# Kernel optimization log

Measured on AMD Instinct MI355X. Metric: run time of the kernel, lower is better.

The kernel has to match this reference:

```python
import jax, jax.numpy as jnp
import numpy as np

WIN = 7
HEADS = 3

def _relative_bias(window_size: int) -> jnp.ndarray:
    # Faithful reproduction of RelativeEmbeddings.__init__ (numpy handles negative
    # indices with wrap-around exactly like torch fancy indexing).
    rng = np.random.default_rng(0)
    B = rng.standard_normal((2 * window_size - 1, 2 * window_size - 1)).astype(np.float32)
    x = np.arange(1, window_size + 1, 1 / window_size)  # length window_size**2
    xi = (x[None, :] - x[:, None]).astype(np.int64)
    y = np.concatenate([np.arange(1, window_size + 1)] * window_size)
    yi = y[None, :] - y[:, None]
    return jnp.asarray(B[xi, yi])  # [w^2, w^2]


def setup_inputs() -> dict:
    key = jax.random.key(0)
    k0, k1, k2 = jax.random.split(key, 3)
    C = 96
    x = jax.random.normal(k0, (64, 3136, C), dtype=jnp.float32)
    w_qkv = jax.random.normal(k1, (C, 3 * C), dtype=jnp.float32) * 0.02
    b_qkv = jnp.zeros((3 * C,), dtype=jnp.float32)
    w_proj = jax.random.normal(k2, (C, C), dtype=jnp.float32) * 0.02
    b_proj = jnp.zeros((C,), dtype=jnp.float32)
    rel_bias = _relative_bias(WIN)
    return {"x": x, "w_qkv": w_qkv, "b_qkv": b_qkv, "w_proj": w_proj,
            "b_proj": b_proj, "rel_bias": rel_bias}


def reference(x, w_qkv, b_qkv, w_proj, b_proj, rel_bias):
    B, L, C = x.shape
    h = w = int(np.sqrt(L))
    m = WIN
    H = HEADS
    E = C // H
    scale = 1.0 / (E ** 0.5)

    qkv = x @ w_qkv + b_qkv                                   # [B, L, 3C]
    # torch rearrange: last dim layout is (H, E, K=3), spatial split into windows
    qkv = qkv.reshape(B, h // m, m, w // m, m, H, E, 3)
    qkv = qkv.transpose(0, 5, 1, 3, 2, 4, 6, 7)               # [B,H,hw,ww,m1,m2,E,3]
    qkv = qkv.reshape(B, H, h // m, w // m, m * m, E, 3)
    q, k, v = qkv[..., 0], qkv[..., 1], qkv[..., 2]           # [B,H,hw,ww,m^2,E]

    scores = jnp.einsum('bhxyqe,bhxyke->bhxyqk', q, k) * scale + rel_bias
    attn = jax.nn.softmax(scores, axis=-1)
    out = jnp.einsum('bhxyqk,bhxyke->bhxyqe', attn, v)        # [B,H,hw,ww,m^2,E]

    out = out.reshape(B, H, h // m, w // m, m, m, E)
    out = out.transpose(0, 2, 4, 3, 5, 1, 6).reshape(B, L, C)  # b (h m1) (w m2) (H E)
    return out @ w_proj + b_proj
```

## Files before the change

### kernel.cpp

```cpp
#include <hip/hip_runtime.h>

typedef unsigned int u32;
typedef __bf16 bf16_t;
typedef bf16_t bf16x8 __attribute__((ext_vector_type(8)));
typedef float f32x4 __attribute__((ext_vector_type(4)));

#define NB 64
#define GH 56
#define CC 96
#define NH 3
#define MM 7
#define WT 49
#define C3 288
#define LL 3136

static constexpr size_t ATTN_OFF = 0;
static constexpr size_t WQ_OFF   = (size_t)NB * LL * CC * 2;
static constexpr size_t WP_OFF   = WQ_OFF + 54 * 1024;
static constexpr size_t BR_OFF   = WP_OFF + 18 * 1024;

static __device__ __forceinline__ unsigned short f2bu(float f) {
    union { bf16_t b; unsigned short u; } c; c.b = (bf16_t)f; return c.u;
}
static __device__ __forceinline__ f32x4 mfma16(bf16x8 a, bf16x8 b, f32x4 c) {
    return __builtin_amdgcn_mfma_f32_16x16x32_bf16(a, b, c, 0, 0, 0);
}

__global__ __launch_bounds__(64) void prep_kernel(
    const float* __restrict__ w_qkv, const float* __restrict__ b_qkv,
    const float* __restrict__ w_proj, char* __restrict__ ws)
{
    const int l = threadIdx.x;
    const int blk = blockIdx.x;
    if (blk < 54) {
        const int h = blk / 18, nt = (blk % 18) / 3, ks = blk % 3;
        const int colp = nt * 16 + (l & 15);
        const int e = colp & 31, wh = colp >> 5;
        const int k0 = ks * 32 + (l >> 4) * 8;
        u32 p[4];
        #pragma unroll
        for (int jj = 0; jj < 4; ++jj) {
            unsigned short a = f2bu(w_qkv[(size_t)(k0 + 2*jj    ) * C3 + h * CC + e * 3 + wh]);
            unsigned short b = f2bu(w_qkv[(size_t)(k0 + 2*jj + 1) * C3 + h * CC + e * 3 + wh]);
            p[jj] = (u32)a | ((u32)b << 16);
        }
        uint4 v; v.x = p[0]; v.y = p[1]; v.z = p[2]; v.w = p[3];
        *(uint4*)(ws + WQ_OFF + ((size_t)blk * 64 + l) * 16) = v;
    } else if (blk < 72) {
        const int idx = blk - 54, nt = idx / 3, ks = idx % 3;
        const int n = nt * 16 + (l & 15);
        const int k0 = ks * 32 + (l >> 4) * 8;
        u32 p[4];
        #pragma unroll
        for (int jj = 0; jj < 4; ++jj) {
            unsigned short a = f2bu(w_proj[(size_t)(k0 + 2*jj    ) * CC + n]);
            unsigned short b = f2bu(w_proj[(size_t)(k0 + 2*jj + 1) * CC + n]);
            p[jj] = (u32)a | ((u32)b << 16);
        }
        uint4 v; v.x = p[0]; v.y = p[1]; v.z = p[2]; v.w = p[3];
        *(uint4*)(ws + WP_OFF + ((size_t)idx * 64 + l) * 16) = v;
    } else {
        float* br = (float*)(ws + BR_OFF);
        for (int i = l; i < C3; i += 64) {
            int h = i / CC, c = i % CC;
            br[i] = b_qkv[h * CC + (c & 31) * 3 + (c >> 5)];
        }
    }
}

__global__ __launch_bounds__(256, 3) void attn_kernel(
    const float* __restrict__ x, const float* __restrict__ rel_bias,
    const char* __restrict__ wsro, bf16_t* __restrict__ attn_out)
{
    __shared__ bf16_t s_x [64][104];
    __shared__ bf16_t s_q [64][40];
    __shared__ bf16_t s_k [64][40];
    __shared__ bf16_t s_vT[32][72];
    __shared__ bf16_t s_p [64][72];
    __shared__ float  s_bias[WT][50];

    const int tid = threadIdx.x;
    const int l = tid & 63, w = tid >> 6;
    const int ln = l & 15, quad = l >> 4;
    const int b = blockIdx.x >> 6, win = blockIdx.x & 63;
    const int wy = win >> 3, wx = win & 7;
    const int q0 = 16 * w + quad * 4;

    for (int i = tid; i < 1536; i += 256) {
        const int t = i / 24, c4 = (i % 24) * 4;
        float4 xv = {0.f, 0.f, 0.f, 0.f};
        if (t < WT) {
            const int grow = (wy * MM + t / MM) * GH + wx * MM + t % MM;
            xv = *(const float4*)&x[((size_t)b * LL + grow) * CC + c4];
        }
        ushort4 pv;
        pv.x = f2bu(xv.x); pv.y = f2bu(xv.y); pv.z = f2bu(xv.z); pv.w = f2bu(xv.w);
        *(ushort4*)((char*)&s_x[0][0] + t * 208 + c4 * 2) = pv;
    }
    for (int i = tid; i < WT * WT; i += 256) s_bias[i / WT][i % WT] = rel_bias[i];
    __syncthreads();

    const char* wq = wsro + WQ_OFF;
    const float* br = (const float*)(wsro + BR_OFF);
    const float scale = 0.17677669529663687f;

    for (int h = 0; h < NH; ++h) {
        const char* sxrow = (const char*)&s_x[0][0] + (16 * w + ln) * 208 + quad * 16;
        bf16x8 a0 = *(const bf16x8*)(sxrow);
        bf16x8 a1 = *(const bf16x8*)(sxrow + 64);
        bf16x8 a2 = *(const bf16x8*)(sxrow + 128);
        #pragma unroll
        for (int nt = 0; nt < 6; ++nt) {
            const char* wqp = wq + ((size_t)(h * 18 + nt * 3)) * 1024 + (size_t)l * 16;
            bf16x8 b0 = *(const bf16x8*)(wqp);
            bf16x8 b1 = *(const bf16x8*)(wqp + 1024);
            bf16x8 b2 = *(const bf16x8*)(wqp + 2048);
            f32x4 acc = {0.f, 0.f, 0.f, 0.f};
            acc = mfma16(a0, b0, acc);
            acc = mfma16(a1, b1, acc);
            acc = mfma16(a2, b2, acc);
            const float bias = br[h * CC + nt * 16 + ln];
            if (nt < 4) {
                bf16_t* dst = (nt < 2) ? &s_q[0][0] : &s_k[0][0];
                const int col = (nt & 1) * 16 + ln;
                #pragma unroll
                for (int r = 0; r < 4; ++r) {
                    float v = acc[r] + bias;
                    float ov = __shfl_xor(v, 1);
                    if (!(l & 1))
                        *(u32*)((char*)dst + (q0 + r) * 80 + col * 2) =
                            (u32)f2bu(v) | ((u32)f2bu(ov) << 16);
                }
            } else {
                const int e = (nt - 4) * 16 + ln;
                uint2 pk;
                pk.x = (u32)f2bu(acc[0] + bias) | ((u32)f2bu(acc[1] + bias) << 16);
                pk.y = (u32)f2bu(acc[2] + bias) | ((u32)f2bu(acc[3] + bias) << 16);
                *(uint2*)((char*)&s_vT[0][0] + e * 144 + q0 * 2) = pk;
            }
        }
        __syncthreads();

        bf16x8 qa = *(const bf16x8*)((const char*)&s_q[0][0] + (16 * w + ln) * 80 + quad * 16);
        float sv[4][4];
        #pragma unroll
        for (int nt = 0; nt < 4; ++nt) {
            bf16x8 kb = *(const bf16x8*)((const char*)&s_k[0][0] + (16 * nt + ln) * 80 + quad * 16);
            f32x4 z = {0.f, 0.f, 0.f, 0.f};
            z = mfma16(qa, kb, z);
            const int kk = 16 * nt + ln;
            #pragma unroll
            for (int r = 0; r < 4; ++r) {
                const int q = q0 + r;
                float bb = (q < WT && kk < WT) ? s_bias[q][kk] : 0.f;
                float v = z[r] * scale + bb;
                sv[nt][r] = (kk < WT) ? v : -1e30f;
            }
        }
        #pragma unroll
        for (int r = 0; r < 4; ++r) {
            float m = fmaxf(fmaxf(sv[0][r], sv[1][r]), fmaxf(sv[2][r], sv[3][r]));
            m = fmaxf(m, __shfl_xor(m, 1));
            m = fmaxf(m, __shfl_xor(m, 2));
            m = fmaxf(m, __shfl_xor(m, 4));
            m = fmaxf(m, __shfl_xor(m, 8));
            float s = 0.f;
            #pragma unroll
            for (int nt = 0; nt < 4; ++nt) { sv[nt][r] = __expf(sv[nt][r] - m); s += sv[nt][r]; }
            s += __shfl_xor(s, 1);
            s += __shfl_xor(s, 2);
            s += __shfl_xor(s, 4);
            s += __shfl_xor(s, 8);
            const float inv = 1.f / s;
            #pragma unroll
            for (int nt = 0; nt < 4; ++nt) sv[nt][r] *= inv;
        }
        #pragma unroll
        for (int nt = 0; nt < 4; ++nt) {
            const int kk = 16 * nt + ln;
            #pragma unroll
            for (int r = 0; r < 4; ++r) {
                float v = sv[nt][r];
                float ov = __shfl_xor(v, 1);
                if (!(l & 1))
                    *(u32*)((char*)&s_p[0][0] + (q0 + r) * 144 + kk * 2) =
                        (u32)f2bu(v) | ((u32)f2bu(ov) << 16);
            }
        }
        __syncthreads();

        const char* sprow = (const char*)&s_p[0][0] + (16 * w + ln) * 144 + quad * 16;
        bf16x8 pa0 = *(const bf16x8*)(sprow);
        bf16x8 pa1 = *(const bf16x8*)(sprow + 64);
        #pragma unroll
        for (int nt = 0; nt < 2; ++nt) {
            const char* svr = (const char*)&s_vT[0][0] + (16 * nt + ln) * 144 + quad * 16;
            bf16x8 vb0 = *(const bf16x8*)(svr);
            bf16x8 vb1 = *(const bf16x8*)(svr + 64);
            f32x4 z = {0.f, 0.f, 0.f, 0.f};
            z = mfma16(pa0, vb0, z);
            z = mfma16(pa1, vb1, z);
            const int c = h * 32 + nt * 16 + ln;
            #pragma unroll
            for (int r = 0; r < 4; ++r) {
                const int t = q0 + r;
                float v = z[r];
                float ov = __shfl_xor(v, 1);
                if (!(l & 1) && t < WT) {
                    const int grow = (wy * MM + t / MM) * GH + wx * MM + t % MM;
                    const size_t off = ((size_t)b * LL + grow) * CC + c;
                    *(u32*)((char*)attn_out + off * 2) = (u32)f2bu(v) | ((u32)f2bu(ov) << 16);
                }
            }
        }
        __syncthreads();
    }
}

__global__ __launch_bounds__(256) void proj_kernel(
    const bf16_t* __restrict__ A, const char* __restrict__ wsro,
    const float* __restrict__ b_proj, float* __restrict__ out)
{
    __shared__ bf16_t s_a[128][104];
    const int tid = threadIdx.x;
    const int l = tid & 63, w = tid >> 6;
    const int ln = l & 15, quad = l >> 4;
    const size_t r0 = (size_t)blockIdx.x * 128;

    for (int i = tid; i < 1536; i += 256) {
        const int row = i / 12, c8 = (i % 12) * 8;
        uint4 v = *(const uint4*)((const char*)A + ((r0 + row) * CC + c8) * 2);
        *(uint4*)((char*)&s_a[0][0] + row * 208 + c8 * 2) = v;
    }
    __syncthreads();

    const char* wp = wsro + WP_OFF;
    bf16x8 af[2][3];
    #pragma unroll
    for (int m2 = 0; m2 < 2; ++m2) {
        const char* sar = (const char*)&s_a[0][0] + (16 * (2 * w + m2) + ln) * 208 + quad * 16;
        af[m2][0] = *(const bf16x8*)(sar);
        af[m2][1] = *(const bf16x8*)(sar + 64);
        af[m2][2] = *(const bf16x8*)(sar + 128);
    }
    #pragma unroll
    for (int nt = 0; nt < 6; ++nt) {
        const char* wpp = wp + (size_t)(nt * 3) * 1024 + (size_t)l * 16;
        bf16x8 b0 = *(const bf16x8*)(wpp);
        bf16x8 b1 = *(const bf16x8*)(wpp + 1024);
        bf16x8 b2 = *(const bf16x8*)(wpp + 2048);
        const float bias = b_proj[nt * 16 + ln];
        #pragma unroll
        for (int m2 = 0; m2 < 2; ++m2) {
            f32x4 acc = {0.f, 0.f, 0.f, 0.f};
            acc = mfma16(af[m2][0], b0, acc);
            acc = mfma16(af[m2][1], b1, acc);
            acc = mfma16(af[m2][2], b2, acc);
            const size_t row0 = r0 + 16 * (2 * w + m2) + quad * 4;
            #pragma unroll
            for (int r = 0; r < 4; ++r)
                out[(row0 + r) * CC + nt * 16 + ln] = acc[r] + bias;
        }
    }
}

extern "C" void kernel_launch(void* const* d_in, const int* in_sizes, int n_in,
                              void* d_out, int out_size, void* d_ws, size_t ws_size,
                              hipStream_t stream)
{
    const float* x      = (const float*)d_in[0];
    const float* w_qkv  = (const float*)d_in[1];
    const float* b_qkv  = (const float*)d_in[2];
    const float* w_proj = (const float*)d_in[3];
    const float* b_proj = (const float*)d_in[4];
    const float* rb     = (const float*)d_in[5];
    char* ws = (char*)d_ws;

    prep_kernel<<<73, 64, 0, stream>>>(w_qkv, b_qkv, w_proj, ws);
    attn_kernel<<<NB * 64, 256, 0, stream>>>(x, rb, ws, (bf16_t*)(ws + ATTN_OFF));
    proj_kernel<<<(NB * LL) / 128, 256, 0, stream>>>(
        (const bf16_t*)(ws + ATTN_OFF), ws, b_proj, (float*)d_out);
}
```

Measured before the change: 272.5 us.

## Fuse output projection into window attention kernel and use 512-thread blocks

Removes the separate projection kernel and the bf16 intermediate attention buffer in global memory. Each window block now accumulates the output projection per head from a shared-memory tile of attention output and writes fp32 results directly. Blocks grow to 8 waves, splitting the N-tiles of the QKV GEMM and P·V across wave halves; only four waves do softmax. This adds an extra shared buffer and a barrier per head, and leaves half the waves idle during the softmax step.

```diff
diff --git a/kernel.cpp b/kernel.cpp
--- a/kernel.cpp
+++ b/kernel.cpp
@@ -14,13 +14,15 @@
 #define C3 288
 #define LL 3136
 
-static constexpr size_t ATTN_OFF = 0;
-static constexpr size_t WQ_OFF   = (size_t)NB * LL * CC * 2;
-static constexpr size_t WP_OFF   = WQ_OFF + 54 * 1024;
-static constexpr size_t BR_OFF   = WP_OFF + 18 * 1024;
+static constexpr size_t WQ_OFF = 0;
+static constexpr size_t WP_OFF = WQ_OFF + 54 * 1024;
+static constexpr size_t BR_OFF = WP_OFF + 18 * 1024;
 
 static __device__ __forceinline__ unsigned short f2bu(float f) {
     union { bf16_t b; unsigned short u; } c; c.b = (bf16_t)f; return c.u;
+}
+static __device__ __forceinline__ u32 pack2(float a, float b) {
+    return (u32)f2bu(a) | ((u32)f2bu(b) << 16);
 }
 static __device__ __forceinline__ f32x4 mfma16(bf16x8 a, bf16x8 b, f32x4 c) {
     return __builtin_amdgcn_mfma_f32_16x16x32_bf16(a, b, c, 0, 0, 0);
@@ -39,11 +41,9 @@
         const int k0 = ks * 32 + (l >> 4) * 8;
         u32 p[4];
         #pragma unroll
-        for (int jj = 0; jj < 4; ++jj) {
-            unsigned short a = f2bu(w_qkv[(size_t)(k0 + 2*jj    ) * C3 + h * CC + e * 3 + wh]);
-            unsigned short b = f2bu(w_qkv[(size_t)(k0 + 2*jj + 1) * C3 + h * CC + e * 3 + wh]);
-            p[jj] = (u32)a | ((u32)b << 16);
-        }
+        for (int jj = 0; jj < 4; ++jj)
+            p[jj] = pack2(w_qkv[(size_t)(k0 + 2*jj    ) * C3 + h * CC + e * 3 + wh],
+                          w_qkv[(size_t)(k0 + 2*jj + 1) * C3 + h * CC + e * 3 + wh]);
         uint4 v; v.x = p[0]; v.y = p[1]; v.z = p[2]; v.w = p[3];
         *(uint4*)(ws + WQ_OFF + ((size_t)blk * 64 + l) * 16) = v;
     } else if (blk < 72) {
@@ -52,11 +52,9 @@
         const int k0 = ks * 32 + (l >> 4) * 8;
         u32 p[4];
         #pragma unroll
-        for (int jj = 0; jj < 4; ++jj) {
-            unsigned short a = f2bu(w_proj[(size_t)(k0 + 2*jj    ) * CC + n]);
-            unsigned short b = f2bu(w_proj[(size_t)(k0 + 2*jj + 1) * CC + n]);
-            p[jj] = (u32)a | ((u32)b << 16);
-        }
+        for (int jj = 0; jj < 4; ++jj)
+            p[jj] = pack2(w_proj[(size_t)(k0 + 2*jj    ) * CC + n],
+                          w_proj[(size_t)(k0 + 2*jj + 1) * CC + n]);
         uint4 v; v.x = p[0]; v.y = p[1]; v.z = p[2]; v.w = p[3];
         *(uint4*)(ws + WP_OFF + ((size_t)idx * 64 + l) * 16) = v;
     } else {
@@ -68,15 +66,17 @@
     }
 }
 
-__global__ __launch_bounds__(256, 3) void attn_kernel(
+__global__ __launch_bounds__(512, 6) void attn_fused_kernel(
     const float* __restrict__ x, const float* __restrict__ rel_bias,
-    const char* __restrict__ wsro, bf16_t* __restrict__ attn_out)
+    const char* __restrict__ wsro, const float* __restrict__ b_proj,
+    float* __restrict__ out)
 {
     __shared__ bf16_t s_x [64][104];
     __shared__ bf16_t s_q [64][40];
     __shared__ bf16_t s_k [64][40];
     __shared__ bf16_t s_vT[32][72];
     __shared__ bf16_t s_p [64][72];
+    __shared__ bf16_t s_o [64][40];
     __shared__ float  s_bias[WT][50];
 
     const int tid = threadIdx.x;
@@ -84,9 +84,11 @@
     const int ln = l & 15, quad = l >> 4;
     const int b = blockIdx.x >> 6, win = blockIdx.x & 63;
     const int wy = win >> 3, wx = win & 7;
-    const int q0 = 16 * w + quad * 4;
-
-    for (int i = tid; i < 1536; i += 256) {
+    const int m  = w & 3;
+    const int hi = w >> 2;
+    const int q0m = 16 * m + quad * 4;
+
+    for (int i = tid; i < 1536; i += 512) {
         const int t = i / 24, c4 = (i % 24) * 4;
         float4 xv = {0.f, 0.f, 0.f, 0.f};
         if (t < WT) {
@@ -97,28 +99,30 @@
         pv.x = f2bu(xv.x); pv.y = f2bu(xv.y); pv.z = f2bu(xv.z); pv.w = f2bu(xv.w);
         *(ushort4*)((char*)&s_x[0][0] + t * 208 + c4 * 2) = pv;
     }
-    for (int i = tid; i < WT * WT; i += 256) s_bias[i / WT][i % WT] = rel_bias[i];
+    for (int i = tid; i < WT * WT; i += 512) s_bias[i / WT][i % WT] = rel_bias[i];
     __syncthreads();
 
     const char* wq = wsro + WQ_OFF;
+    const char* wp = wsro + WP_OFF;
     const float* br = (const float*)(wsro + BR_OFF);
     const float scale = 0.17677669529663687f;
 
+    f32x4 accp[3] = {{0.f,0.f,0.f,0.f},{0.f,0.f,0.f,0.f},{0.f,0.f,0.f,0.f}};
+
+    const char* sxrow = (const char*)&s_x[0][0] + (16 * m + ln) * 208 + quad * 16;
+    const bf16x8 xa0 = *(const bf16x8*)(sxrow);
+    const bf16x8 xa1 = *(const bf16x8*)(sxrow + 64);
+    const bf16x8 xa2 = *(const bf16x8*)(sxrow + 128);
+
     for (int h = 0; h < NH; ++h) {
-        const char* sxrow = (const char*)&s_x[0][0] + (16 * w + ln) * 208 + quad * 16;
-        bf16x8 a0 = *(const bf16x8*)(sxrow);
-        bf16x8 a1 = *(const bf16x8*)(sxrow + 64);
-        bf16x8 a2 = *(const bf16x8*)(sxrow + 128);
-        #pragma unroll
-        for (int nt = 0; nt < 6; ++nt) {
-            const char* wqp = wq + ((size_t)(h * 18 + nt * 3)) * 1024 + (size_t)l * 16;
-            bf16x8 b0 = *(const bf16x8*)(wqp);
-            bf16x8 b1 = *(const bf16x8*)(wqp + 1024);
-            bf16x8 b2 = *(const bf16x8*)(wqp + 2048);
+        #pragma unroll
+        for (int jj = 0; jj < 3; ++jj) {
+            const int nt = hi + 2 * jj;
+            const char* wqp = wq + (size_t)(h * 18 + nt * 3) * 1024 + (size_t)l * 16;
             f32x4 acc = {0.f, 0.f, 0.f, 0.f};
-            acc = mfma16(a0, b0, acc);
-            acc = mfma16(a1, b1, acc);
-            acc = mfma16(a2, b2, acc);
+            acc = mfma16(xa0, *(const bf16x8*)(wqp       ), acc);
+            acc = mfma16(xa1, *(const bf16x8*)(wqp + 1024), acc);
+            acc = mfma16(xa2, *(const bf16x8*)(wqp + 2048), acc);
             const float bias = br[h * CC + nt * 16 + ln];
             if (nt < 4) {
                 bf16_t* dst = (nt < 2) ? &s_q[0][0] : &s_k[0][0];
@@ -128,138 +132,110 @@
                     float v = acc[r] + bias;
                     float ov = __shfl_xor(v, 1);
                     if (!(l & 1))
-                        *(u32*)((char*)dst + (q0 + r) * 80 + col * 2) =
-                            (u32)f2bu(v) | ((u32)f2bu(ov) << 16);
+                        *(u32*)((char*)dst + (q0m + r) * 80 + col * 2) = pack2(v, ov);
                 }
             } else {
                 const int e = (nt - 4) * 16 + ln;
                 uint2 pk;
-                pk.x = (u32)f2bu(acc[0] + bias) | ((u32)f2bu(acc[1] + bias) << 16);
-                pk.y = (u32)f2bu(acc[2] + bias) | ((u32)f2bu(acc[3] + bias) << 16);
-                *(uint2*)((char*)&s_vT[0][0] + e * 144 + q0 * 2) = pk;
+                pk.x = pack2(acc[0] + bias, acc[1] + bias);
+                pk.y = pack2(acc[2] + bias, acc[3] + bias);
+                *(uint2*)((char*)&s_vT[0][0] + e * 144 + q0m * 2) = pk;
             }
         }
         __syncthreads();
 
-        bf16x8 qa = *(const bf16x8*)((const char*)&s_q[0][0] + (16 * w + ln) * 80 + quad * 16);
-        float sv[4][4];
-        #pragma unroll
-        for (int nt = 0; nt < 4; ++nt) {
-            bf16x8 kb = *(const bf16x8*)((const char*)&s_k[0][0] + (16 * nt + ln) * 80 + quad * 16);
-            f32x4 z = {0.f, 0.f, 0.f, 0.f};
-            z = mfma16(qa, kb, z);
-            const int kk = 16 * nt + ln;
+        if (w < 4) {
+            const bf16x8 qa = *(const bf16x8*)((const char*)&s_q[0][0] + (16 * m + ln) * 80 + quad * 16);
+            float sv[4][4];
+            #pragma unroll
+            for (int nt = 0; nt < 4; ++nt) {
+                const bf16x8 kb = *(const bf16x8*)((const char*)&s_k[0][0] + (16 * nt + ln) * 80 + quad * 16);
+                f32x4 z = {0.f, 0.f, 0.f, 0.f};
+                z = mfma16(qa, kb, z);
+                const int kk = 16 * nt + ln;
+                #pragma unroll
+                for (int r = 0; r < 4; ++r) {
+                    const int q = q0m + r;
+                    float bb = (q < WT && kk < WT) ? s_bias[q][kk] : 0.f;
+                    sv[nt][r] = (kk < WT) ? z[r] * scale + bb : -1e30f;
+                }
+            }
             #pragma unroll
             for (int r = 0; r < 4; ++r) {
-                const int q = q0 + r;
-                float bb = (q < WT && kk < WT) ? s_bias[q][kk] : 0.f;
-                float v = z[r] * scale + bb;
-                sv[nt][r] = (kk < WT) ? v : -1e30f;
-            }
-        }
-        #pragma unroll
-        for (int r = 0; r < 4; ++r) {
-            float m = fmaxf(fmaxf(sv[0][r], sv[1][r]), fmaxf(sv[2][r], sv[3][r]));
-            m = fmaxf(m, __shfl_xor(m, 1));
-            m = fmaxf(m, __shfl_xor(m, 2));
-            m = fmaxf(m, __shfl_xor(m, 4));
-            m = fmaxf(m, __shfl_xor(m, 8));
-            float s = 0.f;
-            #pragma unroll
-            for (int nt = 0; nt < 4; ++nt) { sv[nt][r] = __expf(sv[nt][r] - m); s += sv[nt][r]; }
-            s += __shfl_xor(s, 1);
-            s += __shfl_xor(s, 2);
-            s += __shfl_xor(s, 4);
-            s += __shfl_xor(s, 8);
-            const float inv = 1.f / s;
-            #pragma unroll
-            for (int nt = 0; nt < 4; ++nt) sv[nt][r] *= inv;
-        }
-        #pragma unroll
-        for (int nt = 0; nt < 4; ++nt) {
-            const int kk = 16 * nt + ln;
-            #pragma unroll
-            for (int r = 0; r < 4; ++r) {
-                float v = sv[nt][r];
-                float ov = __shfl_xor(v, 1);
-                if (!(l & 1))
-                    *(u32*)((char*)&s_p[0][0] + (q0 + r) * 144 + kk * 2) =
-                        (u32)f2bu(v) | ((u32)f2bu(ov) << 16);
+                float mx = fmaxf(fmaxf(sv[0][r], sv[1][r]), fmaxf(sv[2][r], sv[3][r]));
+                mx = fmaxf(mx, __shfl_xor(mx, 1));
+                mx = fmaxf(mx, __shfl_xor(mx, 2));
+                mx = fmaxf(mx, __shfl_xor(mx, 4));
+                mx = fmaxf(mx, __shfl_xor(mx, 8));
+                float s = 0.f;
+                #pragma unroll
+                for (int nt = 0; nt < 4; ++nt) { sv[nt][r] = __expf(sv[nt][r] - mx); s += sv[nt][r]; }
+                s += __shfl_xor(s, 1);
+                s += __shfl_xor(s, 2);
+                s += __shfl_xor(s, 4);
+                s += __shfl_xor(s, 8);
+                const float inv = 1.f / s;
+                #pragma unroll
+                for (int nt = 0; nt < 4; ++nt) sv[nt][r] *= inv;
+            }
+            #pragma unroll
+            for (int nt = 0; nt < 4; ++nt) {
+                const int kk = 16 * nt + ln;
+                #pragma unroll
+                for (int r = 0; r < 4; ++r) {
+                    float v = sv[nt][r];
+                    float ov = __shfl_xor(v, 1);
+                    if (!(l & 1))
+                        *(u32*)((char*)&s_p[0][0] + (q0m + r) * 144 + kk * 2) = pack2(v, ov);
+                }
             }
         }
         __syncthreads();
 
-        const char* sprow = (const char*)&s_p[0][0] + (16 * w + ln) * 144 + quad * 16;
-        bf16x8 pa0 = *(const bf16x8*)(sprow);
-        bf16x8 pa1 = *(const bf16x8*)(sprow + 64);
-        #pragma unroll
-        for (int nt = 0; nt < 2; ++nt) {
-            const char* svr = (const char*)&s_vT[0][0] + (16 * nt + ln) * 144 + quad * 16;
-            bf16x8 vb0 = *(const bf16x8*)(svr);
-            bf16x8 vb1 = *(const bf16x8*)(svr + 64);
+        {
+            const char* sprow = (const char*)&s_p[0][0] + (16 * m + ln) * 144 + quad * 16;
+            const bf16x8 pa0 = *(const bf16x8*)(sprow);
+            const bf16x8 pa1 = *(const bf16x8*)(sprow + 64);
+            const char* svr = (const char*)&s_vT[0][0] + (16 * hi + ln) * 144 + quad * 16;
+            const bf16x8 vb0 = *(const bf16x8*)(svr);
+            const bf16x8 vb1 = *(const bf16x8*)(svr + 64);
             f32x4 z = {0.f, 0.f, 0.f, 0.f};
             z = mfma16(pa0, vb0, z);
             z = mfma16(pa1, vb1, z);
-            const int c = h * 32 + nt * 16 + ln;
+            const int col = hi * 16 + ln;
             #pragma unroll
             for (int r = 0; r < 4; ++r) {
-                const int t = q0 + r;
                 float v = z[r];
                 float ov = __shfl_xor(v, 1);
-                if (!(l & 1) && t < WT) {
-                    const int grow = (wy * MM + t / MM) * GH + wx * MM + t % MM;
-                    const size_t off = ((size_t)b * LL + grow) * CC + c;
-                    *(u32*)((char*)attn_out + off * 2) = (u32)f2bu(v) | ((u32)f2bu(ov) << 16);
-                }
+                if (!(l & 1))
+                    *(u32*)((char*)&s_o[0][0] + (q0m + r) * 80 + col * 2) = pack2(v, ov);
             }
         }
         __syncthreads();
-    }
-}
-
-__global__ __launch_bounds__(256) void proj_kernel(
-    const bf16_t* __restrict__ A, const char* __restrict__ wsro,
-    const float* __restrict__ b_proj, float* __restrict__ out)
-{
-    __shared__ bf16_t s_a[128][104];
-    const int tid = threadIdx.x;
-    const int l = tid & 63, w = tid >> 6;
-    const int ln = l & 15, quad = l >> 4;
-    const size_t r0 = (size_t)blockIdx.x * 128;
-
-    for (int i = tid; i < 1536; i += 256) {
-        const int row = i / 12, c8 = (i % 12) * 8;
-        uint4 v = *(const uint4*)((const char*)A + ((r0 + row) * CC + c8) * 2);
-        *(uint4*)((char*)&s_a[0][0] + row * 208 + c8 * 2) = v;
-    }
-    __syncthreads();
-
-    const char* wp = wsro + WP_OFF;
-    bf16x8 af[2][3];
+
+        {
+            const bf16x8 oa = *(const bf16x8*)((const char*)&s_o[0][0] + (16 * m + ln) * 80 + quad * 16);
+            #pragma unroll
+            for (int jj = 0; jj < 3; ++jj) {
+                const int nt = hi + 2 * jj;
+                const char* wpp = wp + (size_t)(nt * 3 + h) * 1024 + (size_t)l * 16;
+                accp[jj] = mfma16(oa, *(const bf16x8*)(wpp), accp[jj]);
+            }
+        }
+    }
+
     #pragma unroll
-    for (int m2 = 0; m2 < 2; ++m2) {
-        const char* sar = (const char*)&s_a[0][0] + (16 * (2 * w + m2) + ln) * 208 + quad * 16;
-        af[m2][0] = *(const bf16x8*)(sar);
-        af[m2][1] = *(const bf16x8*)(sar + 64);
-        af[m2][2] = *(const bf16x8*)(sar + 128);
-    }
-    #pragma unroll
-    for (int nt = 0; nt < 6; ++nt) {
-        const char* wpp = wp + (size_t)(nt * 3) * 1024 + (size_t)l * 16;
-        bf16x8 b0 = *(const bf16x8*)(wpp);
-        bf16x8 b1 = *(const bf16x8*)(wpp + 1024);
-        bf16x8 b2 = *(const bf16x8*)(wpp + 2048);
-        const float bias = b_proj[nt * 16 + ln];
-        #pragma unroll
-        for (int m2 = 0; m2 < 2; ++m2) {
-            f32x4 acc = {0.f, 0.f, 0.f, 0.f};
-            acc = mfma16(af[m2][0], b0, acc);
-            acc = mfma16(af[m2][1], b1, acc);
-            acc = mfma16(af[m2][2], b2, acc);
-            const size_t row0 = r0 + 16 * (2 * w + m2) + quad * 4;
-            #pragma unroll
-            for (int r = 0; r < 4; ++r)
-                out[(row0 + r) * CC + nt * 16 + ln] = acc[r] + bias;
+    for (int jj = 0; jj < 3; ++jj) {
+        const int nt = hi + 2 * jj;
+        const int col = nt * 16 + ln;
+        const float bp = b_proj[col];
+        #pragma unroll
+        for (int r = 0; r < 4; ++r) {
+            const int t = q0m + r;
+            if (t < WT) {
+                const int grow = (wy * MM + t / MM) * GH + wx * MM + t % MM;
+                out[((size_t)b * LL + grow) * CC + col] = accp[jj][r] + bp;
+            }
         }
     }
 }
@@ -277,7 +253,5 @@
     char* ws = (char*)d_ws;
 
     prep_kernel<<<73, 64, 0, stream>>>(w_qkv, b_qkv, w_proj, ws);
-    attn_kernel<<<NB * 64, 256, 0, stream>>>(x, rb, ws, (bf16_t*)(ws + ATTN_OFF));
-    proj_kernel<<<(NB * LL) / 128, 256, 0, stream>>>(
-        (const bf16_t*)(ws + ATTN_OFF), ws, b_proj, (float*)d_out);
-}
+    attn_fused_kernel<<<NB * 64, 512, 0, stream>>>(x, rb, ws, b_proj, (float*)d_out);
+}
```

Result: slower. 326.2 us (+19.7%).
